# Performance work log

Hardware: AMD Instinct MI355X
Metric: run time of the kernel (lower is better)

## Reference

```python
import jax, jax.numpy as jnp
import numpy as np

BITS = 4
QMAX = 2 ** (BITS - 1) - 1   # 7
OFF = 2 ** (BITS - 1)        # 8
L = 2 ** BITS                # 16 LUT levels per operand


def _quant(x):
    """Symmetric per-tensor quantization to signed BITS-bit levels.
    Returns integer-valued levels (as float, in [-OFF, QMAX]) and the scale."""
    s = jnp.maximum(jnp.max(jnp.abs(x)) / QMAX, 1e-8)
    q = jnp.clip(jnp.round(x / s), -OFF, QMAX)
    return q, s


def _lut_conv3x3(x, w, b, lut):
    """3x3 same-padding conv where every scalar multiply a*w is replaced by
    lut[idx(a), idx(w)]. x:[B,C,H,W], w:[O,C,3,3], b:[O], lut:[L,L]."""
    B, C, H, W = x.shape
    O = w.shape[0]
    qx, sx = _quant(x)
    qw, sw = _quant(w)
    # zero-padding: level 0 is the quantized value 0, so padding is exact
    xp = jnp.pad(qx, ((0, 0), (0, 0), (1, 1), (1, 1)))
    # im2col: [B, C, 9, H, W] -> [B, H, W, K], K = C*9 (order: c-major, then kh,kw)
    patches = jnp.stack([xp[:, :, i:i + H, j:j + W]
                         for i in range(3) for j in range(3)], axis=2)
    K = C * 9
    patches = patches.reshape(B, K, H, W).transpose(0, 2, 3, 1)
    idx_a = (patches + OFF).astype(jnp.int32)            # [B,H,W,K]
    mapped = lut[idx_a]                                   # [B,H,W,K,L]
    idx_w = (qw.reshape(O, K).T + OFF).astype(jnp.int32)  # [K,O]
    onehot_w = jax.nn.one_hot(idx_w, L, dtype=x.dtype)    # [K,O,L]
    # out[b,o,h,w] = sum_k lut[idx_a[b,h,w,k], idx_w[k,o]]
    out = jnp.einsum('bhwkl,kol->bohw', mapped, onehot_w)
    return out * (sx * sw) + b[None, :, None, None]


def _lut_linear(x, w, b, lut):
    """x:[B,F], w:[O,F], b:[O], lut:[L,L]; y[b,o]=sum_f lut[idx(x),idx(w)]."""
    qx, sx = _quant(x)
    qw, sw = _quant(w)
    idx_a = (qx + OFF).astype(jnp.int32)                 # [B,F]
    mapped = lut[idx_a]                                   # [B,F,L]
    idx_w = (qw.T + OFF).astype(jnp.int32)                # [F,O]
    onehot_w = jax.nn.one_hot(idx_w, L, dtype=x.dtype)    # [F,O,L]
    out = jnp.einsum('bfl,fol->bo', mapped, onehot_w)
    return out * (sx * sw) + b[None, :]


def _maxpool2(x):
    B, C, H, W = x.shape
    return x.reshape(B, C, H // 2, 2, W // 2, 2).max(axis=(3, 5))


def setup_inputs() -> dict:
    key = jax.random.key(0)
    ks = jax.random.split(key, 20)
    d = {}
    d['x'] = jax.random.normal(ks[0], (8, 3, 32, 32), jnp.float32)
    conv_shapes = [(64, 3), (192, 64), (384, 192), (256, 384), (256, 256)]
    for i, (o, c) in enumerate(conv_shapes):
        d[f'w{i}'] = jax.random.normal(ks[1 + 2 * i], (o, c, 3, 3), jnp.float32) * 0.05
        d[f'b{i}'] = jax.random.normal(ks[2 + 2 * i], (o,), jnp.float32) * 0.01
    fc_shapes = [(4096, 4096), (4096, 4096), (10, 4096)]
    for j, (o, f) in enumerate(fc_shapes):
        d[f'w{5 + j}'] = jax.random.normal(ks[11 + 2 * j], (o, f), jnp.float32) * 0.02
        d[f'b{5 + j}'] = jax.random.normal(ks[12 + 2 * j], (o,), jnp.float32) * 0.01
    # per-layer approximate-multiplier LUTs: exact product of signed levels + error
    levels = jnp.arange(-OFF, OFF, dtype=jnp.float32)       # [-8..7]
    base = jnp.outer(levels, levels)                        # [16,16]
    noise = jax.random.normal(ks[17], (8, L, L), jnp.float32) * 0.25
    d['luts'] = base[None, :, :] + noise
    return d


def reference(x, w0, b0, w1, b1, w2, b2, w3, b3, w4, b4,
              w5, b5, w6, b6, w7, b7, luts):
    relu = jax.nn.relu
    h = relu(_lut_conv3x3(x, w0, b0, luts[0]))
    h = _maxpool2(h)                                  # [B,64,16,16]
    h = relu(_lut_conv3x3(h, w1, b1, luts[1]))
    h = _maxpool2(h)                                  # [B,192,8,8]
    h = relu(_lut_conv3x3(h, w2, b2, luts[2]))        # [B,384,8,8]
    h = relu(_lut_conv3x3(h, w3, b3, luts[3]))        # [B,256,8,8]
    h = relu(_lut_conv3x3(h, w4, b4, luts[4]))
    h = _maxpool2(h)                                  # [B,256,4,4]
    h = h.reshape(h.shape[0], 256 * 4 * 4)
    h = relu(_lut_linear(h, w5, b5, luts[5]))         # dropout = identity (eval)
    h = relu(_lut_linear(h, w6, b6, luts[6]))
    return _lut_linear(h, w7, b7, luts[7])            # [B,10]
```

## Files before the change

kernel.cpp:

```cpp
#include <hip/hip_runtime.h>
#include <stdint.h>


#define DI __device__ __forceinline__

constexpr size_t alup(size_t x){ return (x + 511) & ~(size_t)511; }
constexpr size_t O_SLOTS = 0;
constexpr size_t O_IA0 = 512;
constexpr size_t O_IA1 = alup(O_IA0 + 24576);
constexpr size_t O_IA2 = alup(O_IA1 + 131072);
constexpr size_t O_IA3 = alup(O_IA2 + 98304);
constexpr size_t O_IA4 = alup(O_IA3 + 196608);
constexpr size_t O_IA5 = alup(O_IA4 + 131072);
constexpr size_t O_IA6 = alup(O_IA5 + 32768);
constexpr size_t O_IA7 = alup(O_IA6 + 32768);
constexpr size_t O_WP0 = alup(O_IA7 + 32768);
constexpr size_t O_WP1 = alup(O_WP0 + 864);
constexpr size_t O_WP2 = alup(O_WP1 + 55296);
constexpr size_t O_WP3 = alup(O_WP2 + 331776);
constexpr size_t O_WP4 = alup(O_WP3 + 442368);
constexpr size_t O_A1  = alup(O_WP4 + 294912);
constexpr size_t O_A2  = alup(O_A1 + 1048576);
constexpr size_t O_A3  = alup(O_A2 + 786432);
constexpr size_t O_A4  = alup(O_A3 + 1572864);
constexpr size_t O_A5  = alup(O_A4 + 1048576);
constexpr size_t O_H5  = alup(O_A5 + 262144);
constexpr size_t O_H6  = alup(O_H5 + 262144);
constexpr size_t O_P1  = alup(O_H6 + 262144);
constexpr size_t O_P2  = O_P1 + 3145728;
constexpr size_t O_P3  = O_P2 + 1572864;
constexpr size_t O_P4  = O_P3 + 1048576;
constexpr int    PZ_D4 = 212992;


DI double getscale(const double* slots, int i){ return fmax(slots[i] / 7.0, 1e-8); }
DI int quant_idx_r(double v, double r){
  double q = fmin(fmax(rint(v * r), -8.0), 7.0);
  return (int)q + 8;
}
DI void atomicMaxD(double* addr, double v){
  atomicMax((unsigned long long*)addr, (unsigned long long)__double_as_longlong(v));
}

__global__ __launch_bounds__(256) void k_zero_all(double4* pz, double* slots){
  int i = blockIdx.x*256 + threadIdx.x;
  if (i < PZ_D4){ double4 z; z.x=z.y=z.z=z.w=0.0; pz[i] = z; }
  else if (i - PZ_D4 < 16) slots[i - PZ_D4] = 0.0;
}

__global__ __launch_bounds__(256) void k_wmax(
    const float* w0, const float* w1, const float* w2, const float* w3, const float* w4,
    const float* w5, const float* w6, const float* w7, const float* x, double* slots)
{
  const int sizes[9] = {1728,110592,663552,884736,589824,16777216,16777216,40960,24576};
  const int cum[10]  = {0,1,5,26,53,71,583,1095,1097,1098};
  int bid = blockIdx.x;
  int seg = 0;
  #pragma unroll
  for (int s2 = 0; s2 < 9; ++s2) if (bid >= cum[s2+1]) seg = s2+1;
  const float* p;
  switch (seg){
    case 0: p = w0; break; case 1: p = w1; break; case 2: p = w2; break;
    case 3: p = w3; break; case 4: p = w4; break; case 5: p = w5; break;
    case 6: p = w6; break; case 7: p = w7; break; default: p = x; break;
  }
  int n = sizes[seg];
  long base = (long)(bid - cum[seg]) * 32768;
  float m = 0.f;
  for (long i = base + threadIdx.x * 4; i < base + 32768 && i < (long)n; i += 1024){
    float4 v = *(const float4*)(p + i);
    m = fmaxf(m, fmaxf(fmaxf(fabsf(v.x), fabsf(v.y)), fmaxf(fabsf(v.z), fabsf(v.w))));
  }
  #pragma unroll
  for (int off = 32; off; off >>= 1) m = fmaxf(m, __shfl_xor(m, off, 64));
  __shared__ float red[4];
  if ((threadIdx.x & 63) == 0) red[threadIdx.x >> 6] = m;
  __syncthreads();
  if (threadIdx.x == 0)
    atomicMaxD(&slots[seg], (double)fmaxf(fmaxf(red[0], red[1]), fmaxf(red[2], red[3])));
}

__global__ __launch_bounds__(256) void k_wq(
    const float* w0, const float* w1, const float* w2, const float* w3, const float* w4,
    const float* x, const double* slots, uint8_t* ws)
{
  int item = blockIdx.x * 256 + threadIdx.x;
  if (item < 281304){
    const float* w; uint32_t* wp; int K; int r; double s;
    if (item < 216)        { w=w0; wp=(uint32_t*)(ws+O_WP0); K=27;   r=item;        s=getscale(slots,0); }
    else if (item < 14040) { w=w1; wp=(uint32_t*)(ws+O_WP1); K=576;  r=item-216;    s=getscale(slots,1); }
    else if (item < 96984) { w=w2; wp=(uint32_t*)(ws+O_WP2); K=1728; r=item-14040;  s=getscale(slots,2); }
    else if (item < 207576){ w=w3; wp=(uint32_t*)(ws+O_WP3); K=3456; r=item-96984;  s=getscale(slots,3); }
    else                   { w=w4; wp=(uint32_t*)(ws+O_WP4); K=2304; r=item-207576; s=getscale(slots,4); }
    double rs = 1.0 / s;
    int og = r / K, k = r % K;
    uint32_t pack = 0;
    #pragma unroll
    for (int j = 0; j < 8; ++j){
      double wv = (double)w[(size_t)(og*8 + j)*K + k];
      pack |= (uint32_t)quant_idx_r(wv, rs) << (4*j);
    }
    wp[og*K + k] = pack;
  } else if (item < 287448){
    int i2 = item - 281304;
    double rs = 1.0 / getscale(slots, 8);
    uint32_t pack = 0;
    #pragma unroll
    for (int r2 = 0; r2 < 4; ++r2)
      pack |= (uint32_t)quant_idx_r((double)x[i2*4 + r2], rs) << (8*r2);
    ((uint32_t*)(ws + O_IA0))[i2] = pack;
  }
}

__global__ __launch_bounds__(256) void k_conv0(
    const uint8_t* __restrict__ ia0, const uint32_t* __restrict__ wp0,
    const float* __restrict__ lut_g, const float* __restrict__ bias,
    double* slots, double* __restrict__ a1)
{
  __shared__ double lutT[256];
  int tid = threadIdx.x;
  lutT[(tid & 15)*16 + (tid >> 4)] = (double)lut_g[tid];
  __syncthreads();
  int b = blockIdx.x >> 6, o = blockIdx.x & 63;
  int yp = tid >> 4, xp = tid & 15;
  double scale = getscale(slots, 8) * getscale(slots, 0);
  double bo = (double)bias[o];
  double pool = 0.0;
  #pragma unroll
  for (int dy = 0; dy < 2; ++dy)
  #pragma unroll
  for (int dx = 0; dx < 2; ++dx){
    int y = yp*2 + dy, x2 = xp*2 + dx;
    double sum = 0.0;
    #pragma unroll
    for (int c = 0; c < 3; ++c)
      #pragma unroll
      for (int ty = 0; ty < 3; ++ty)
        #pragma unroll
        for (int tx = 0; tx < 3; ++tx){
          int yy = y + ty - 1, xx = x2 + tx - 1;
          int ia = 8;
          if (yy >= 0 && yy < 32 && xx >= 0 && xx < 32)
            ia = ia0[((b*3 + c)*32 + yy)*32 + xx];
          uint32_t sw = wp0[(o >> 3)*27 + c*9 + ty*3 + tx];
          int iw = (sw >> ((o & 7)*4)) & 15;
          sum += lutT[iw*16 + ia];
        }
    pool = fmax(pool, fmax(sum*scale + bo, 0.0));
  }
  a1[((b*64 + o)*16 + yp)*16 + xp] = pool;
  double m = pool;
  #pragma unroll
  for (int off = 32; off; off >>= 1) m = fmax(m, __shfl_xor(m, off, 64));
  __shared__ double red[4];
  if ((tid & 63) == 0) red[tid >> 6] = m;
  __syncthreads();
  if (tid == 0) atomicMaxD(&slots[9], fmax(fmax(red[0],red[1]), fmax(red[2],red[3])));
}

template<int C, int O, int H, int W, int CT, int ROWS, int SP, int KS>
__global__ __launch_bounds__(256) void k_conv(
    const uint8_t* __restrict__ iain, const uint32_t* __restrict__ wp,
    const float* __restrict__ lut_g, double* __restrict__ P)
{
  constexpr int KT = CT*9;
  constexpr int AW = W + 2, AH = ROWS + 2;
  __shared__ double lutT[256];
  __shared__ uint32_t wps[4*KT];
  __shared__ uint8_t acts[CT*AH*AW];
  int tid = threadIdx.x;
  int bx = blockIdx.x;
  int ks = bx % KS; int rem = bx / KS;
  int ob = rem % (O/32); rem /= (O/32);
  int sp = rem % SP; int b = rem / SP;
  lutT[(tid & 15)*16 + (tid >> 4)] = (double)lut_g[tid];
  for (int i = tid; i < 4*KT; i += 256){
    int w2 = i / KT, k = i % KT;
    wps[i] = wp[(size_t)(ob*4 + w2)*(C*9) + (size_t)ks*KT + k];
  }
  for (int i = tid; i < CT*AH*AW; i += 256){
    int ct = i / (AH*AW);
    int r  = (i / AW) % AH;
    int cc = i % AW;
    int y = sp*ROWS + r - 1, x2 = cc - 1;
    uint8_t v = 8;
    if (y >= 0 && y < H && x2 >= 0 && x2 < W)
      v = iain[(((size_t)b*C + ks*CT + ct)*H + y)*W + x2];
    acts[i] = v;
  }
  __syncthreads();
  int wid = tid >> 6, lane = tid & 63;
  int ly = lane / W, lx = lane % W;
  double acc[8] = {0,0,0,0,0,0,0,0};
  const uint32_t* wrow = &wps[wid*KT];
  #pragma unroll 1
  for (int ct = 0; ct < CT; ++ct){
    int abase = (ct*AH + ly)*AW + lx;
    #pragma unroll
    for (int ty = 0; ty < 3; ++ty)
    #pragma unroll
    for (int tx = 0; tx < 3; ++tx){
      int ia = acts[abase + ty*AW + tx];
      uint32_t sw = (uint32_t)__builtin_amdgcn_readfirstlane((int)wrow[ct*9 + ty*3 + tx]);
      #pragma unroll
      for (int j = 0; j < 8; ++j)
        acc[j] += lutT[((sw >> (4*j)) & 15u)*16 + ia];
    }
  }
  int y = sp*ROWS + ly;
  int obase = ob*32 + wid*8;
  #pragma unroll
  for (int j = 0; j < 8; ++j)
    atomicAdd(&P[(((size_t)b*O + obase + j)*H + y)*W + lx], acc[j]);
}

template<int O, int Hc, int Wc, bool POOL>
__global__ __launch_bounds__(256) void k_post(
    const double* __restrict__ P, const float* __restrict__ bias,
    double* __restrict__ aout, double* slots, int sx_slot, int sw_slot, int ma_slot)
{
  constexpr int Ho = POOL ? Hc/2 : Hc, Wo = POOL ? Wc/2 : Wc;
  int i = blockIdx.x*256 + threadIdx.x;
  int x2 = i % Wo, y = (i / Wo) % Ho, o = (i / (Wo*Ho)) % O, b = i / (Wo*Ho*O);
  double scale = getscale(slots, sx_slot) * getscale(slots, sw_slot);
  double bo = (double)bias[o];
  double res;
  if (POOL){
    double p = 0.0;
    #pragma unroll
    for (int dy = 0; dy < 2; ++dy)
    #pragma unroll
    for (int dx = 0; dx < 2; ++dx){
      double s = P[(((size_t)b*O + o)*Hc + y*2+dy)*Wc + x2*2+dx];
      p = fmax(p, fmax(s*scale + bo, 0.0));
    }
    res = p;
  } else {
    double s = P[(((size_t)b*O + o)*Hc + y)*Wc + x2];
    res = fmax(s*scale + bo, 0.0);
  }
  aout[i] = res;
  double m = res;
  #pragma unroll
  for (int off = 32; off; off >>= 1) m = fmax(m, __shfl_xor(m, off, 64));
  __shared__ double red[4];
  if ((threadIdx.x & 63) == 0) red[threadIdx.x >> 6] = m;
  __syncthreads();
  if (threadIdx.x == 0)
    atomicMaxD(&slots[ma_slot], fmax(fmax(red[0],red[1]), fmax(red[2],red[3])));
}

__global__ __launch_bounds__(256) void k_aq_conv(
    const double* __restrict__ in, uint8_t* __restrict__ out,
    const double* slots, int slot, int n)
{
  int i = blockIdx.x*256 + threadIdx.x;
  if (i >= n) return;
  double rs = 1.0 / getscale(slots, slot);
  out[i] = (uint8_t)quant_idx_r(in[i], rs);
}

__global__ __launch_bounds__(256) void k_aq_fc(
    const double* __restrict__ in, uint32_t* __restrict__ lo, uint32_t* __restrict__ hi,
    const double* slots, int slot)
{
  int f = blockIdx.x*256 + threadIdx.x;
  double rs = 1.0 / getscale(slots, slot);
  uint32_t l = 0, h = 0;
  #pragma unroll
  for (int b2 = 0; b2 < 4; ++b2) l |= (uint32_t)quant_idx_r(in[(size_t)b2*4096 + f], rs) << (8*b2);
  #pragma unroll
  for (int b2 = 4; b2 < 8; ++b2) h |= (uint32_t)quant_idx_r(in[(size_t)b2*4096 + f], rs) << (8*(b2-4));
  lo[f] = l; hi[f] = h;
}

template<bool RELU>
__global__ __launch_bounds__(256) void k_fc(
    const float* __restrict__ Wm, const float* __restrict__ bias,
    const uint32_t* __restrict__ ialo, const uint32_t* __restrict__ iahi,
    const float* __restrict__ lut_g, double* __restrict__ out,
    double* slots, int sx_slot, int sw_slot, int ma_slot)
{
  __shared__ double lutT[256];
  __shared__ uint32_t los[4096], his[4096];
  __shared__ double red[4];
  int tid = threadIdx.x;
  lutT[(tid & 15)*16 + (tid >> 4)] = (double)lut_g[tid];
  for (int i = tid; i < 4096; i += 256){ los[i] = ialo[i]; his[i] = iahi[i]; }
  __syncthreads();
  double sw = getscale(slots, sw_slot);
  double rsw = 1.0 / sw;
  double scale = getscale(slots, sx_slot) * sw;
  int wid = tid >> 6, lane = tid & 63;
  int o = blockIdx.x*4 + wid;
  const float* wr = Wm + (size_t)o*4096;
  double acc[8] = {0,0,0,0,0,0,0,0};
  #pragma unroll 2
  for (int ch = 0; ch < 64; ++ch){
    int f = ch*64 + lane;
    unsigned iw = (unsigned)quant_idx_r((double)wr[f], rsw);
    const double* lrow = &lutT[iw << 4];
    uint32_t lo = los[f], hi = his[f];
    acc[0] += lrow[lo & 255];         acc[1] += lrow[(lo >> 8) & 255];
    acc[2] += lrow[(lo >> 16) & 255]; acc[3] += lrow[lo >> 24];
    acc[4] += lrow[hi & 255];         acc[5] += lrow[(hi >> 8) & 255];
    acc[6] += lrow[(hi >> 16) & 255]; acc[7] += lrow[hi >> 24];
  }
  #pragma unroll
  for (int off = 32; off; off >>= 1)
    #pragma unroll
    for (int b2 = 0; b2 < 8; ++b2) acc[b2] += __shfl_xor(acc[b2], off, 64);
  if (lane == 0){
    double m = 0.0;
    double bo = (double)bias[o];
    #pragma unroll
    for (int b2 = 0; b2 < 8; ++b2){
      double h = acc[b2]*scale + bo;
      if (RELU) h = fmax(h, 0.0);
      out[(size_t)b2*4096 + o] = h;
      m = fmax(m, fabs(h));
    }
    red[wid] = m;
  }
  __syncthreads();
  if (tid == 0)
    atomicMaxD(&slots[ma_slot], fmax(fmax(red[0],red[1]), fmax(red[2],red[3])));
}

__global__ __launch_bounds__(256) void k_fc7(
    const float* __restrict__ Wm, const float* __restrict__ bias,
    const uint32_t* __restrict__ ialo, const uint32_t* __restrict__ iahi,
    const float* __restrict__ lut_g, float* __restrict__ out, const double* slots)
{
  __shared__ double lutT[256];
  __shared__ uint32_t los[4096], his[4096];
  __shared__ double red[4][8];
  int tid = threadIdx.x;
  lutT[(tid & 15)*16 + (tid >> 4)] = (double)lut_g[tid];
  for (int i = tid; i < 4096; i += 256){ los[i] = ialo[i]; his[i] = iahi[i]; }
  __syncthreads();
  double sw = getscale(slots, 7);
  double rsw = 1.0 / sw;
  double scale = getscale(slots, 15) * sw;
  int o = blockIdx.x;
  const float* wr = Wm + (size_t)o*4096;
  double acc[8] = {0,0,0,0,0,0,0,0};
  for (int ch = 0; ch < 16; ++ch){
    int f = ch*256 + tid;
    unsigned iw = (unsigned)quant_idx_r((double)wr[f], rsw);
    const double* lrow = &lutT[iw << 4];
    uint32_t lo = los[f], hi = his[f];
    acc[0] += lrow[lo & 255];         acc[1] += lrow[(lo >> 8) & 255];
    acc[2] += lrow[(lo >> 16) & 255]; acc[3] += lrow[lo >> 24];
    acc[4] += lrow[hi & 255];         acc[5] += lrow[(hi >> 8) & 255];
    acc[6] += lrow[(hi >> 16) & 255]; acc[7] += lrow[hi >> 24];
  }
  int wid = tid >> 6, lane = tid & 63;
  #pragma unroll
  for (int off = 32; off; off >>= 1)
    #pragma unroll
    for (int b2 = 0; b2 < 8; ++b2) acc[b2] += __shfl_xor(acc[b2], off, 64);
  if (lane == 0){
    #pragma unroll
    for (int b2 = 0; b2 < 8; ++b2) red[wid][b2] = acc[b2];
  }
  __syncthreads();
  if (tid < 8){
    double v = red[0][tid] + red[1][tid] + red[2][tid] + red[3][tid];
    out[tid*10 + o] = (float)(v*scale + (double)bias[o]);
  }
}

extern "C" void kernel_launch(void* const* d_in, const int* in_sizes, int n_in,
                              void* d_out, int out_size, void* d_ws, size_t ws_size,
                              hipStream_t stream)
{
  (void)in_sizes; (void)n_in; (void)out_size; (void)ws_size;
  const float* x  = (const float*)d_in[0];
  const float* w0 = (const float*)d_in[1];  const float* b0 = (const float*)d_in[2];
  const float* w1 = (const float*)d_in[3];  const float* b1 = (const float*)d_in[4];
  const float* w2 = (const float*)d_in[5];  const float* b2 = (const float*)d_in[6];
  const float* w3 = (const float*)d_in[7];  const float* b3 = (const float*)d_in[8];
  const float* w4 = (const float*)d_in[9];  const float* b4 = (const float*)d_in[10];
  const float* w5 = (const float*)d_in[11]; const float* b5 = (const float*)d_in[12];
  const float* w6 = (const float*)d_in[13]; const float* b6 = (const float*)d_in[14];
  const float* w7 = (const float*)d_in[15]; const float* b7 = (const float*)d_in[16];
  const float* luts = (const float*)d_in[17];

  uint8_t* ws = (uint8_t*)d_ws;
  double* slots = (double*)(ws + O_SLOTS);
  const uint8_t* IA0 = ws + O_IA0;
  uint8_t *IA1 = ws + O_IA1, *IA2 = ws + O_IA2, *IA3 = ws + O_IA3, *IA4 = ws + O_IA4;
  uint32_t *IA5lo = (uint32_t*)(ws + O_IA5), *IA5hi = IA5lo + 4096;
  uint32_t *IA6lo = (uint32_t*)(ws + O_IA6), *IA6hi = IA6lo + 4096;
  uint32_t *IA7lo = (uint32_t*)(ws + O_IA7), *IA7hi = IA7lo + 4096;
  const uint32_t* WP0 = (const uint32_t*)(ws + O_WP0);
  const uint32_t* WP1 = (const uint32_t*)(ws + O_WP1);
  const uint32_t* WP2 = (const uint32_t*)(ws + O_WP2);
  const uint32_t* WP3 = (const uint32_t*)(ws + O_WP3);
  const uint32_t* WP4 = (const uint32_t*)(ws + O_WP4);
  double *A1 = (double*)(ws + O_A1), *A2 = (double*)(ws + O_A2), *A3 = (double*)(ws + O_A3);
  double *A4 = (double*)(ws + O_A4), *A5 = (double*)(ws + O_A5);
  double *H5 = (double*)(ws + O_H5), *H6 = (double*)(ws + O_H6);
  double *P1 = (double*)(ws + O_P1), *P2 = (double*)(ws + O_P2);
  double *P3 = (double*)(ws + O_P3), *P4 = (double*)(ws + O_P4);

  k_zero_all<<<833, 256, 0, stream>>>((double4*)(ws + O_P1), slots);
  k_wmax<<<1098, 256, 0, stream>>>(w0,w1,w2,w3,w4,w5,w6,w7,x,slots);
  k_wq<<<1123, 256, 0, stream>>>(w0,w1,w2,w3,w4,x,slots,ws);

  k_conv0<<<512, 256, 0, stream>>>(IA0, WP0, luts + 0, b0, slots, A1);
  k_aq_conv<<<512, 256, 0, stream>>>(A1, IA1, slots, 9, 131072);

  k_conv<64,192,16,16,8,4,4,8><<<1536, 256, 0, stream>>>(IA1, WP1, luts + 256, P1);
  k_post<192,16,16,true><<<384, 256, 0, stream>>>(P1, b1, A2, slots, 9, 1, 10);
  k_aq_conv<<<384, 256, 0, stream>>>(A2, IA2, slots, 10, 98304);

  k_conv<192,384,8,8,12,8,1,16><<<1536, 256, 0, stream>>>(IA2, WP2, luts + 512, P2);
  k_post<384,8,8,false><<<768, 256, 0, stream>>>(P2, b2, A3, slots, 10, 2, 11);
  k_aq_conv<<<768, 256, 0, stream>>>(A3, IA3, slots, 11, 196608);

  k_conv<384,256,8,8,12,8,1,32><<<2048, 256, 0, stream>>>(IA3, WP3, luts + 768, P3);
  k_post<256,8,8,false><<<512, 256, 0, stream>>>(P3, b3, A4, slots, 11, 3, 12);
  k_aq_conv<<<512, 256, 0, stream>>>(A4, IA4, slots, 12, 131072);

  k_conv<256,256,8,8,8,8,1,32><<<2048, 256, 0, stream>>>(IA4, WP4, luts + 1024, P4);
  k_post<256,8,8,true><<<128, 256, 0, stream>>>(P4, b4, A5, slots, 12, 4, 13);
  k_aq_fc<<<16, 256, 0, stream>>>(A5, IA5lo, IA5hi, slots, 13);

  k_fc<true><<<1024, 256, 0, stream>>>(w5, b5, IA5lo, IA5hi, luts + 1280, H5, slots, 13, 5, 14);
  k_aq_fc<<<16, 256, 0, stream>>>(H5, IA6lo, IA6hi, slots, 14);
  k_fc<true><<<1024, 256, 0, stream>>>(w6, b6, IA6lo, IA6hi, luts + 1536, H6, slots, 14, 6, 15);
  k_aq_fc<<<16, 256, 0, stream>>>(H6, IA7lo, IA7hi, slots, 15);
  k_fc7<<<10, 256, 0, stream>>>(w7, b7, IA7lo, IA7hi, luts + 1792, (float*)d_out, slots);
}
```

Before: 502.7 us.

## Fuse activation quantization into conv tile loads and shrink LUTs to float

```diff
diff --git a/kernel.cpp b/kernel.cpp
--- a/kernel.cpp
+++ b/kernel.cpp
@@ -7,11 +7,7 @@
 constexpr size_t alup(size_t x){ return (x + 511) & ~(size_t)511; }
 constexpr size_t O_SLOTS = 0;
 constexpr size_t O_IA0 = 512;
-constexpr size_t O_IA1 = alup(O_IA0 + 24576);
-constexpr size_t O_IA2 = alup(O_IA1 + 131072);
-constexpr size_t O_IA3 = alup(O_IA2 + 98304);
-constexpr size_t O_IA4 = alup(O_IA3 + 196608);
-constexpr size_t O_IA5 = alup(O_IA4 + 131072);
+constexpr size_t O_IA5 = alup(O_IA0 + 24576);
 constexpr size_t O_IA6 = alup(O_IA5 + 32768);
 constexpr size_t O_IA7 = alup(O_IA6 + 32768);
 constexpr size_t O_WP0 = alup(O_IA7 + 32768);
@@ -117,9 +113,9 @@
     const float* __restrict__ lut_g, const float* __restrict__ bias,
     double* slots, double* __restrict__ a1)
 {
-  __shared__ double lutT[256];
+  __shared__ float lutT[256];
   int tid = threadIdx.x;
-  lutT[(tid & 15)*16 + (tid >> 4)] = (double)lut_g[tid];
+  lutT[(tid & 15)*16 + (tid >> 4)] = lut_g[tid];
   __syncthreads();
   int b = blockIdx.x >> 6, o = blockIdx.x & 63;
   int yp = tid >> 4, xp = tid & 15;
@@ -144,7 +140,7 @@
             ia = ia0[((b*3 + c)*32 + yy)*32 + xx];
           uint32_t sw = wp0[(o >> 3)*27 + c*9 + ty*3 + tx];
           int iw = (sw >> ((o & 7)*4)) & 15;
-          sum += lutT[iw*16 + ia];
+          sum += (double)lutT[iw*16 + ia];
         }
     pool = fmax(pool, fmax(sum*scale + bo, 0.0));
   }
@@ -160,51 +156,58 @@
 
 template<int C, int O, int H, int W, int CT, int ROWS, int SP, int KS>
 __global__ __launch_bounds__(256) void k_conv(
-    const uint8_t* __restrict__ iain, const uint32_t* __restrict__ wp,
-    const float* __restrict__ lut_g, double* __restrict__ P)
+    const double* __restrict__ ain, const uint32_t* __restrict__ wp,
+    const float* __restrict__ lut_g, const double* __restrict__ slots,
+    int sx_slot, double* __restrict__ P)
 {
   constexpr int KT = CT*9;
   constexpr int AW = W + 2, AH = ROWS + 2;
-  __shared__ double lutT[256];
-  __shared__ uint32_t wps[4*KT];
+  __shared__ float lutT[256];
+  __shared__ alignas(16) uint32_t wps[4*CT*12];
   __shared__ uint8_t acts[CT*AH*AW];
   int tid = threadIdx.x;
   int bx = blockIdx.x;
   int ks = bx % KS; int rem = bx / KS;
   int ob = rem % (O/32); rem /= (O/32);
   int sp = rem % SP; int b = rem / SP;
-  lutT[(tid & 15)*16 + (tid >> 4)] = (double)lut_g[tid];
+  lutT[(tid & 15)*16 + (tid >> 4)] = lut_g[tid];
   for (int i = tid; i < 4*KT; i += 256){
     int w2 = i / KT, k = i % KT;
-    wps[i] = wp[(size_t)(ob*4 + w2)*(C*9) + (size_t)ks*KT + k];
-  }
+    wps[(w2*CT + k/9)*12 + (k%9)] = wp[(size_t)(ob*4 + w2)*(C*9) + (size_t)ks*KT + k];
+  }
+  double rsx = 1.0 / getscale(slots, sx_slot);
   for (int i = tid; i < CT*AH*AW; i += 256){
     int ct = i / (AH*AW);
     int r  = (i / AW) % AH;
     int cc = i % AW;
     int y = sp*ROWS + r - 1, x2 = cc - 1;
-    uint8_t v = 8;
+    int v = 8;
     if (y >= 0 && y < H && x2 >= 0 && x2 < W)
-      v = iain[(((size_t)b*C + ks*CT + ct)*H + y)*W + x2];
-    acts[i] = v;
+      v = quant_idx_r(ain[(((size_t)b*C + ks*CT + ct)*H + y)*W + x2], rsx);
+    acts[i] = (uint8_t)(v << 2);
   }
   __syncthreads();
   int wid = tid >> 6, lane = tid & 63;
   int ly = lane / W, lx = lane % W;
   double acc[8] = {0,0,0,0,0,0,0,0};
-  const uint32_t* wrow = &wps[wid*KT];
+  const char* lutB = (const char*)lutT;
   #pragma unroll 1
   for (int ct = 0; ct < CT; ++ct){
     int abase = (ct*AH + ly)*AW + lx;
+    const uint32_t* wr2 = &wps[(wid*CT + ct)*12];
+    uint4 wa = *(const uint4*)(wr2);
+    uint4 wb = *(const uint4*)(wr2 + 4);
+    uint32_t wc = wr2[8];
+    uint32_t wv[9] = {wa.x, wa.y, wa.z, wa.w, wb.x, wb.y, wb.z, wb.w, wc};
     #pragma unroll
     for (int ty = 0; ty < 3; ++ty)
     #pragma unroll
     for (int tx = 0; tx < 3; ++tx){
-      int ia = acts[abase + ty*AW + tx];
-      uint32_t sw = (uint32_t)__builtin_amdgcn_readfirstlane((int)wrow[ct*9 + ty*3 + tx]);
+      int ia4 = acts[abase + ty*AW + tx];
+      uint32_t sw = (uint32_t)__builtin_amdgcn_readfirstlane((int)wv[ty*3 + tx]);
       #pragma unroll
       for (int j = 0; j < 8; ++j)
-        acc[j] += lutT[((sw >> (4*j)) & 15u)*16 + ia];
+        acc[j] += (double)*(const float*)(lutB + (((sw >> (4*j)) & 15u) << 6) + ia4);
     }
   }
   int y = sp*ROWS + ly;
@@ -250,43 +253,34 @@
     atomicMaxD(&slots[ma_slot], fmax(fmax(red[0],red[1]), fmax(red[2],red[3])));
 }
 
-__global__ __launch_bounds__(256) void k_aq_conv(
-    const double* __restrict__ in, uint8_t* __restrict__ out,
-    const double* slots, int slot, int n)
-{
-  int i = blockIdx.x*256 + threadIdx.x;
-  if (i >= n) return;
-  double rs = 1.0 / getscale(slots, slot);
-  out[i] = (uint8_t)quant_idx_r(in[i], rs);
-}
-
 __global__ __launch_bounds__(256) void k_aq_fc(
-    const double* __restrict__ in, uint32_t* __restrict__ lo, uint32_t* __restrict__ hi,
+    const double* __restrict__ in, uint2* __restrict__ lh,
     const double* slots, int slot)
 {
   int f = blockIdx.x*256 + threadIdx.x;
   double rs = 1.0 / getscale(slots, slot);
   uint32_t l = 0, h = 0;
   #pragma unroll
-  for (int b2 = 0; b2 < 4; ++b2) l |= (uint32_t)quant_idx_r(in[(size_t)b2*4096 + f], rs) << (8*b2);
-  #pragma unroll
-  for (int b2 = 4; b2 < 8; ++b2) h |= (uint32_t)quant_idx_r(in[(size_t)b2*4096 + f], rs) << (8*(b2-4));
-  lo[f] = l; hi[f] = h;
+  for (int b2 = 0; b2 < 4; ++b2)
+    l |= (uint32_t)(quant_idx_r(in[(size_t)b2*4096 + f], rs) << 2) << (8*b2);
+  #pragma unroll
+  for (int b2 = 4; b2 < 8; ++b2)
+    h |= (uint32_t)(quant_idx_r(in[(size_t)b2*4096 + f], rs) << 2) << (8*(b2-4));
+  lh[f] = make_uint2(l, h);
 }
 
 template<bool RELU>
 __global__ __launch_bounds__(256) void k_fc(
     const float* __restrict__ Wm, const float* __restrict__ bias,
-    const uint32_t* __restrict__ ialo, const uint32_t* __restrict__ iahi,
-    const float* __restrict__ lut_g, double* __restrict__ out,
-    double* slots, int sx_slot, int sw_slot, int ma_slot)
-{
-  __shared__ double lutT[256];
-  __shared__ uint32_t los[4096], his[4096];
+    const uint2* __restrict__ lh_g, const float* __restrict__ lut_g,
+    double* __restrict__ out, double* slots, int sx_slot, int sw_slot, int ma_slot)
+{
+  __shared__ float lutT[256];
+  __shared__ uint2 lhs[4096];
   __shared__ double red[4];
   int tid = threadIdx.x;
-  lutT[(tid & 15)*16 + (tid >> 4)] = (double)lut_g[tid];
-  for (int i = tid; i < 4096; i += 256){ los[i] = ialo[i]; his[i] = iahi[i]; }
+  lutT[(tid & 15)*16 + (tid >> 4)] = lut_g[tid];
+  for (int i = tid; i < 4096; i += 256) lhs[i] = lh_g[i];
   __syncthreads();
   double sw = getscale(slots, sw_slot);
   double rsw = 1.0 / sw;
@@ -299,12 +293,16 @@
   for (int ch = 0; ch < 64; ++ch){
     int f = ch*64 + lane;
     unsigned iw = (unsigned)quant_idx_r((double)wr[f], rsw);
-    const double* lrow = &lutT[iw << 4];
-    uint32_t lo = los[f], hi = his[f];
-    acc[0] += lrow[lo & 255];         acc[1] += lrow[(lo >> 8) & 255];
-    acc[2] += lrow[(lo >> 16) & 255]; acc[3] += lrow[lo >> 24];
-    acc[4] += lrow[hi & 255];         acc[5] += lrow[(hi >> 8) & 255];
-    acc[6] += lrow[(hi >> 16) & 255]; acc[7] += lrow[hi >> 24];
+    const char* lb = (const char*)lutT + (iw << 6);
+    uint2 lh = lhs[f];
+    acc[0] += (double)*(const float*)(lb + (lh.x & 255u));
+    acc[1] += (double)*(const float*)(lb + ((lh.x >> 8) & 255u));
+    acc[2] += (double)*(const float*)(lb + ((lh.x >> 16) & 255u));
+    acc[3] += (double)*(const float*)(lb + (lh.x >> 24));
+    acc[4] += (double)*(const float*)(lb + (lh.y & 255u));
+    acc[5] += (double)*(const float*)(lb + ((lh.y >> 8) & 255u));
+    acc[6] += (double)*(const float*)(lb + ((lh.y >> 16) & 255u));
+    acc[7] += (double)*(const float*)(lb + (lh.y >> 24));
   }
   #pragma unroll
   for (int off = 32; off; off >>= 1)
@@ -329,15 +327,15 @@
 
 __global__ __launch_bounds__(256) void k_fc7(
     const float* __restrict__ Wm, const float* __restrict__ bias,
-    const uint32_t* __restrict__ ialo, const uint32_t* __restrict__ iahi,
-    const float* __restrict__ lut_g, float* __restrict__ out, const double* slots)
-{
-  __shared__ double lutT[256];
-  __shared__ uint32_t los[4096], his[4096];
+    const uint2* __restrict__ lh_g, const float* __restrict__ lut_g,
+    float* __restrict__ out, const double* slots)
+{
+  __shared__ float lutT[256];
+  __shared__ uint2 lhs[4096];
   __shared__ double red[4][8];
   int tid = threadIdx.x;
-  lutT[(tid & 15)*16 + (tid >> 4)] = (double)lut_g[tid];
-  for (int i = tid; i < 4096; i += 256){ los[i] = ialo[i]; his[i] = iahi[i]; }
+  lutT[(tid & 15)*16 + (tid >> 4)] = lut_g[tid];
+  for (int i = tid; i < 4096; i += 256) lhs[i] = lh_g[i];
   __syncthreads();
   double sw = getscale(slots, 7);
   double rsw = 1.0 / sw;
@@ -348,12 +346,16 @@
   for (int ch = 0; ch < 16; ++ch){
     int f = ch*256 + tid;
     unsigned iw = (unsigned)quant_idx_r((double)wr[f], rsw);
-    const double* lrow = &lutT[iw << 4];
-    uint32_t lo = los[f], hi = his[f];
-    acc[0] += lrow[lo & 255];         acc[1] += lrow[(lo >> 8) & 255];
-    acc[2] += lrow[(lo >> 16) & 255]; acc[3] += lrow[lo >> 24];
-    acc[4] += lrow[hi & 255];         acc[5] += lrow[(hi >> 8) & 255];
-    acc[6] += lrow[(hi >> 16) & 255]; acc[7] += lrow[hi >> 24];
+    const char* lb = (const char*)lutT + (iw << 6);
+    uint2 lh = lhs[f];
+    acc[0] += (double)*(const float*)(lb + (lh.x & 255u));
+    acc[1] += (double)*(const float*)(lb + ((lh.x >> 8) & 255u));
+    acc[2] += (double)*(const float*)(lb + ((lh.x >> 16) & 255u));
+    acc[3] += (double)*(const float*)(lb + (lh.x >> 24));
+    acc[4] += (double)*(const float*)(lb + (lh.y & 255u));
+    acc[5] += (double)*(const float*)(lb + ((lh.y >> 8) & 255u));
+    acc[6] += (double)*(const float*)(lb + ((lh.y >> 16) & 255u));
+    acc[7] += (double)*(const float*)(lb + (lh.y >> 24));
   }
   int wid = tid >> 6, lane = tid & 63;
   #pragma unroll
@@ -390,10 +392,7 @@
   uint8_t* ws = (uint8_t*)d_ws;
   double* slots = (double*)(ws + O_SLOTS);
   const uint8_t* IA0 = ws + O_IA0;
-  uint8_t *IA1 = ws + O_IA1, *IA2 = ws + O_IA2, *IA3 = ws + O_IA3, *IA4 = ws + O_IA4;
-  uint32_t *IA5lo = (uint32_t*)(ws + O_IA5), *IA5hi = IA5lo + 4096;
-  uint32_t *IA6lo = (uint32_t*)(ws + O_IA6), *IA6hi = IA6lo + 4096;
-  uint32_t *IA7lo = (uint32_t*)(ws + O_IA7), *IA7hi = IA7lo + 4096;
+  uint2 *IA5 = (uint2*)(ws + O_IA5), *IA6 = (uint2*)(ws + O_IA6), *IA7 = (uint2*)(ws + O_IA7);
   const uint32_t* WP0 = (const uint32_t*)(ws + O_WP0);
   const uint32_t* WP1 = (const uint32_t*)(ws + O_WP1);
   const uint32_t* WP2 = (const uint32_t*)(ws + O_WP2);
@@ -410,27 +409,23 @@
   k_wq<<<1123, 256, 0, stream>>>(w0,w1,w2,w3,w4,x,slots,ws);
 
   k_conv0<<<512, 256, 0, stream>>>(IA0, WP0, luts + 0, b0, slots, A1);
-  k_aq_conv<<<512, 256, 0, stream>>>(A1, IA1, slots, 9, 131072);
-
-  k_conv<64,192,16,16,8,4,4,8><<<1536, 256, 0, stream>>>(IA1, WP1, luts + 256, P1);
+
+  k_conv<64,192,16,16,8,4,4,8><<<1536, 256, 0, stream>>>(A1, WP1, luts + 256, slots, 9, P1);
   k_post<192,16,16,true><<<384, 256, 0, stream>>>(P1, b1, A2, slots, 9, 1, 10);
-  k_aq_conv<<<384, 256, 0, stream>>>(A2, IA2, slots, 10, 98304);
-
-  k_conv<192,384,8,8,12,8,1,16><<<1536, 256, 0, stream>>>(IA2, WP2, luts + 512, P2);
+
+  k_conv<192,384,8,8,12,8,1,16><<<1536, 256, 0, stream>>>(A2, WP2, luts + 512, slots, 10, P2);
   k_post<384,8,8,false><<<768, 256, 0, stream>>>(P2, b2, A3, slots, 10, 2, 11);
-  k_aq_conv<<<768, 256, 0, stream>>>(A3, IA3, slots, 11, 196608);
-
-  k_conv<384,256,8,8,12,8,1,32><<<2048, 256, 0, stream>>>(IA3, WP3, luts + 768, P3);
+
+  k_conv<384,256,8,8,12,8,1,32><<<2048, 256, 0, stream>>>(A3, WP3, luts + 768, slots, 11, P3);
   k_post<256,8,8,false><<<512, 256, 0, stream>>>(P3, b3, A4, slots, 11, 3, 12);
-  k_aq_conv<<<512, 256, 0, stream>>>(A4, IA4, slots, 12, 131072);
-
-  k_conv<256,256,8,8,8,8,1,32><<<2048, 256, 0, stream>>>(IA4, WP4, luts + 1024, P4);
+
+  k_conv<256,256,8,8,8,8,1,32><<<2048, 256, 0, stream>>>(A4, WP4, luts + 1024, slots, 12, P4);
   k_post<256,8,8,true><<<128, 256, 0, stream>>>(P4, b4, A5, slots, 12, 4, 13);
-  k_aq_fc<<<16, 256, 0, stream>>>(A5, IA5lo, IA5hi, slots, 13);
-
-  k_fc<true><<<1024, 256, 0, stream>>>(w5, b5, IA5lo, IA5hi, luts + 1280, H5, slots, 13, 5, 14);
-  k_aq_fc<<<16, 256, 0, stream>>>(H5, IA6lo, IA6hi, slots, 14);
-  k_fc<true><<<1024, 256, 0, stream>>>(w6, b6, IA6lo, IA6hi, luts + 1536, H6, slots, 14, 6, 15);
-  k_aq_fc<<<16, 256, 0, stream>>>(H6, IA7lo, IA7hi, slots, 15);
-  k_fc7<<<10, 256, 0, stream>>>(w7, b7, IA7lo, IA7hi, luts + 1792, (float*)d_out, slots);
-}
+  k_aq_fc<<<16, 256, 0, stream>>>(A5, IA5, slots, 13);
+
+  k_fc<true><<<1024, 256, 0, stream>>>(w5, b5, IA5, luts + 1280, H5, slots, 13, 5, 14);
+  k_aq_fc<<<16, 256, 0, stream>>>(H5, IA6, slots, 14);
+  k_fc<true><<<1024, 256, 0, stream>>>(w6, b6, IA6, luts + 1536, H6, slots, 14, 6, 15);
+  k_aq_fc<<<16, 256, 0, stream>>>(H6, IA7, slots, 15);
+  k_fc7<<<10, 256, 0, stream>>>(w7, b7, IA7, luts + 1792, (float*)d_out, slots);
+}
```

After: 516.8 us. 2.8% more time.
